# Optimization experiments

Hardware: AMD Instinct MI355X
Metric: run time of the kernel (lower is better)

The kernel has to match this reference:

```python
import math
import jax, jax.numpy as jnp
import numpy as np

T, N, D = 8, 1024, 128  # num_timestamps, tot_nodes, node_input_size

def setup_inputs() -> dict:
    key = jax.random.key(0)
    k1, k2 = jax.random.split(key)
    raw_features = jax.random.normal(k1, (T, N, D), dtype=jnp.float32)
    adj = jax.random.randint(k2, (N, N), 0, 2, dtype=jnp.int32)
    return {"raw_features": raw_features, "adj": adj}

def reference(raw_features, adj):
    t, n, d = raw_features.shape
    scale = 1.0 / math.sqrt(d)
    # --- GAT: adjacency-masked self-attention per timestamp ---
    scores = jnp.einsum('tnd,tmd->tnm', raw_features, raw_features) * scale  # [T,N,N]
    masked = jnp.where(adj[None] > 0, scores, jnp.float32(-1e12))
    attention = jax.nn.softmax(masked, axis=2)
    node_features = jnp.einsum('tnm,tmd->tnd', attention, raw_features)      # [T,N,D]
    # --- temporal scores per node ---
    spatial_features = node_features.transpose(1, 0, 2)                      # [N,T,D]
    temp_scores = jnp.einsum('ntd,nsd->nts', spatial_features, spatial_features) * scale
    spatial_weights = jax.nn.sigmoid(temp_scores)                            # [N,T,T]
    # --- repeat(N,1,1).view(N,N,T,T) == broadcast over leading axis: ST[i,j] = sw[j] ---
    ST = jnp.broadcast_to(spatial_weights[None], (n, n, t, t))               # [N,N,T,T]
    ST = ST.transpose(3, 1, 2, 0)                                            # [T,N,T,N]
    return ST.reshape(t * n, t * n)
```

## Files before the change

### kernel.cpp

```cpp
#include <hip/hip_runtime.h>
#include <hip/hip_bf16.h>
#include <math.h>

#define T 8
#define N 1024
#define D 128

constexpr float SCALE = 0.08838834764831845f;

typedef __attribute__((ext_vector_type(8))) short short8;
typedef __attribute__((ext_vector_type(4))) float floatx4;

#define MFMA16(a, b, c) __builtin_amdgcn_mfma_f32_16x16x32_bf16((a), (b), (c), 0, 0, 0)

__global__ __launch_bounds__(256) void convert_bf16(const float* __restrict__ X,
                                                    ushort* __restrict__ XB,
                                                    ushort* __restrict__ XBT_hi,
                                                    ushort* __restrict__ XBT_lo) {
    const int t  = blockIdx.y;
    const int n0 = blockIdx.x * 64;
    const int tid = threadIdx.x;

    __shared__ ushort Hi[128][66];
    __shared__ ushort Lo[128][66];

    #pragma unroll
    for (int r = 0; r < 8; ++r) {
        int idx = r * 256 + tid;
        int nl  = idx >> 5;
        int c4  = idx & 31;
        float4 v = *(const float4*)(X + ((size_t)t * N + n0 + nl) * D + c4 * 4);
        float vv[4] = {v.x, v.y, v.z, v.w};
        ushort4 o; ushort* op = (ushort*)&o;
        #pragma unroll
        for (int k = 0; k < 4; ++k) {
            __hip_bfloat16 h = __float2bfloat16(vv[k]);
            float hf = __bfloat162float(h);
            __hip_bfloat16 l = __float2bfloat16(vv[k] - hf);
            op[k] = *(ushort*)&h;
            Hi[c4 * 4 + k][nl] = *(ushort*)&h;
            Lo[c4 * 4 + k][nl] = *(ushort*)&l;
        }
        *(ushort4*)(XB + ((size_t)t * N + n0 + nl) * D + c4 * 4) = o;
    }
    __syncthreads();

    const int u  = tid & 31;
    const int dr = tid >> 5;
    #pragma unroll
    for (int p = 0; p < 16; ++p) {
        int d = p * 8 + dr;
        uint hv = *(const uint*)&Hi[d][2 * u];
        uint lv = *(const uint*)&Lo[d][2 * u];
        size_t off = ((size_t)t * D + d) * N + n0 + 2 * u;
        *(uint*)(XBT_hi + off) = hv;
        *(uint*)(XBT_lo + off) = lv;
    }
}

__global__ __launch_bounds__(256) void attn_fused(const ushort* __restrict__ XB,
                                                  const ushort* __restrict__ XBT_hi,
                                                  const ushort* __restrict__ XBT_lo,
                                                  const int* __restrict__ adj,
                                                  float* __restrict__ NF) {
    const int t  = blockIdx.y;
    const int i0 = blockIdx.x * 16;
    const int tid  = threadIdx.x;
    const int wid  = tid >> 6;
    const int lane = tid & 63;
    const int m    = lane & 15;
    const int quad = lane >> 4;
    const int jbase = wid * 256;

    __shared__ ushort Ph[16][1024];
    __shared__ ushort Plo[16][1024];
    float* red = (float*)&Ph[0][0];

    const ushort* Xt = XB + (size_t)t * N * D;

    short8 afrag[4];
    {
        const ushort* pa = Xt + (size_t)(i0 + m) * D + quad * 8;
        #pragma unroll
        for (int kq = 0; kq < 4; ++kq) afrag[kq] = *(const short8*)(pa + kq * 32);
    }

    floatx4 acc[16];
    #pragma unroll
    for (int c = 0; c < 16; ++c) acc[c] = (floatx4){0.f, 0.f, 0.f, 0.f};

    #pragma unroll
    for (int c = 0; c < 16; ++c) {
        const ushort* pb = Xt + (size_t)(jbase + 16 * c + m) * D + quad * 8;
        short8 b0 = *(const short8*)(pb);
        short8 b1 = *(const short8*)(pb + 32);
        short8 b2 = *(const short8*)(pb + 64);
        short8 b3 = *(const short8*)(pb + 96);
        acc[c] = MFMA16(afrag[0], b0, acc[c]);
        acc[c] = MFMA16(afrag[1], b1, acc[c]);
        acc[c] = MFMA16(afrag[2], b2, acc[c]);
        acc[c] = MFMA16(afrag[3], b3, acc[c]);
    }

    #pragma unroll
    for (int q = 0; q < 4; ++q) {
        const int i = i0 + quad * 4 + q;
        const int* arow = adj + (size_t)i * N + jbase + m;
        #pragma unroll
        for (int c = 0; c < 16; ++c) {
            int a = arow[16 * c];
            acc[c][q] = (a != 0) ? acc[c][q] * SCALE : -1e12f;
        }
    }

    float mx[4], inv[4];
    #pragma unroll
    for (int q = 0; q < 4; ++q) {
        float v_ = acc[0][q];
        #pragma unroll
        for (int c = 1; c < 16; ++c) v_ = fmaxf(v_, acc[c][q]);
        v_ = fmaxf(v_, __shfl_xor(v_, 1));
        v_ = fmaxf(v_, __shfl_xor(v_, 2));
        v_ = fmaxf(v_, __shfl_xor(v_, 4));
        v_ = fmaxf(v_, __shfl_xor(v_, 8));
        mx[q] = v_;
    }
    if (m == 0) {
        #pragma unroll
        for (int q = 0; q < 4; ++q) red[wid * 16 + quad * 4 + q] = mx[q];
    }
    __syncthreads();
    #pragma unroll
    for (int q = 0; q < 4; ++q) {
        int r = quad * 4 + q;
        mx[q] = fmaxf(fmaxf(red[r], red[16 + r]), fmaxf(red[32 + r], red[48 + r]));
    }

    float sm[4];
    #pragma unroll
    for (int q = 0; q < 4; ++q) {
        float s_ = 0.f;
        #pragma unroll
        for (int c = 0; c < 16; ++c) {
            float p = __expf(acc[c][q] - mx[q]);
            acc[c][q] = p;
            s_ += p;
        }
        s_ += __shfl_xor(s_, 1);
        s_ += __shfl_xor(s_, 2);
        s_ += __shfl_xor(s_, 4);
        s_ += __shfl_xor(s_, 8);
        sm[q] = s_;
    }
    if (m == 0) {
        #pragma unroll
        for (int q = 0; q < 4; ++q) red[64 + wid * 16 + quad * 4 + q] = sm[q];
    }
    __syncthreads();
    #pragma unroll
    for (int q = 0; q < 4; ++q) {
        int r = quad * 4 + q;
        inv[q] = 1.f / (red[64 + r] + red[80 + r] + red[96 + r] + red[112 + r]);
    }
    __syncthreads();

    #pragma unroll
    for (int q = 0; q < 4; ++q) {
        const int row = quad * 4 + q;
        #pragma unroll
        for (int c = 0; c < 16; ++c) {
            const int col = jbase + 16 * c + m;
            const int sc = ((((col >> 3) ^ (row & 7)) << 3) | (col & 7));
            float p = acc[c][q] * inv[q];
            __hip_bfloat16 h = __float2bfloat16(p);
            float hf = __bfloat162float(h);
            __hip_bfloat16 l = __float2bfloat16(p - hf);
            Ph[row][sc]  = *(ushort*)&h;
            Plo[row][sc] = *(ushort*)&l;
        }
    }
    __syncthreads();

    floatx4 accN[2];
    accN[0] = (floatx4){0.f, 0.f, 0.f, 0.f};
    accN[1] = (floatx4){0.f, 0.f, 0.f, 0.f};
    const int f0 = wid * 32;
    #pragma unroll 4
    for (int kq = 0; kq < 32; ++kq) {
        const int blk = (((kq * 4 + quad) ^ (m & 7)) << 3);
        short8 ah = *(const short8*)&Ph[m][blk];
        short8 al = *(const short8*)&Plo[m][blk];
        #pragma unroll
        for (int nt = 0; nt < 2; ++nt) {
            size_t off = ((size_t)t * D + f0 + nt * 16 + m) * N + kq * 32 + quad * 8;
            short8 bh = *(const short8*)(XBT_hi + off);
            short8 bl = *(const short8*)(XBT_lo + off);
            accN[nt] = MFMA16(ah, bh, accN[nt]);
            accN[nt] = MFMA16(ah, bl, accN[nt]);
            accN[nt] = MFMA16(al, bh, accN[nt]);
        }
    }

    float* NFt = NF + (size_t)t * N * D;
    #pragma unroll
    for (int nt = 0; nt < 2; ++nt)
        #pragma unroll
        for (int q = 0; q < 4; ++q)
            NFt[(size_t)(i0 + quad * 4 + q) * D + f0 + nt * 16 + m] = accN[nt][q];
}

__global__ __launch_bounds__(256) void expand_fused(const float* __restrict__ NF,
                                                    float* __restrict__ out) {
    const int row = blockIdx.x;
    const int b = row >> 10, j = row & 1023;
    const int tid = threadIdx.x;

    __shared__ float F[T][D + 4];
    __shared__ float w[T];

    {
        int a = tid >> 5, c4 = (tid & 31) * 4;
        *(float4*)(&F[a][c4]) = *(const float4*)(NF + ((size_t)a * N + j) * D + c4);
    }
    __syncthreads();

    if (tid < T) {
        float s = 0.f;
        #pragma unroll
        for (int d4 = 0; d4 < 32; ++d4) {
            float4 fa = *(const float4*)(&F[tid][d4 * 4]);
            float4 fb = *(const float4*)(&F[b][d4 * 4]);
            s += fa.x * fb.x + fa.y * fb.y + fa.z * fb.z + fa.w * fb.w;
        }
        w[tid] = 1.f / (1.f + __expf(-s * SCALE));
    }
    __syncthreads();

    floatx4* orow = (floatx4*)(out + (size_t)row * (T * N));
    #pragma unroll
    for (int a = 0; a < T; ++a) {
        float wv = w[a];
        floatx4 v = {wv, wv, wv, wv};
        __builtin_nontemporal_store(v, orow + a * 256 + tid);
    }
}

extern "C" void kernel_launch(void* const* d_in, const int* in_sizes, int n_in,
                              void* d_out, int out_size, void* d_ws, size_t ws_size,
                              hipStream_t stream) {
    const float* X   = (const float*)d_in[0];
    const int*   adj = (const int*)d_in[1];
    float* out = (float*)d_out;

    float*  NF     = (float*)d_ws;
    ushort* XB     = (ushort*)(NF + (size_t)T * N * D);
    ushort* XBT_hi = XB + (size_t)T * N * D;
    ushort* XBT_lo = XBT_hi + (size_t)T * N * D;

    convert_bf16<<<dim3(N / 64, T), 256, 0, stream>>>(X, XB, XBT_hi, XBT_lo);
    attn_fused<<<dim3(N / 16, T), 256, 0, stream>>>(XB, XBT_hi, XBT_lo, adj, NF);
    expand_fused<<<dim3(T * N), 256, 0, stream>>>(NF, out);
}
```

Before: 320.1 us.

## Pack adjacency into bitmasks and software-pipeline B-operand loads in attention

A new kernel packs the int32 adjacency matrix into 16-bit masks, so the attention kernel reads the mask as a few vector loads instead of 64 scattered int loads per thread for every timestamp. The QK^T loop double-buffers the B fragments, and the PV loop prefetches XBT hi/lo fragments three iterations ahead, issuing the first ones before the softmax. The kernel now has launch bounds allowing 2 blocks per CU. The extra register pressure from the prefetch buffers could cause spills, and the kernel adds a small launch and workspace buffer. The total time is likely dominated by the 256 MB output write in expand_fused, which limits how much the attention changes can matter.

```diff
diff --git a/kernel.cpp b/kernel.cpp
--- a/kernel.cpp
+++ b/kernel.cpp
@@ -58,11 +58,28 @@
     }
 }
 
-__global__ __launch_bounds__(256) void attn_fused(const ushort* __restrict__ XB,
-                                                  const ushort* __restrict__ XBT_hi,
-                                                  const ushort* __restrict__ XBT_lo,
-                                                  const int* __restrict__ adj,
-                                                  float* __restrict__ NF) {
+__global__ __launch_bounds__(256) void pack_adj(const int* __restrict__ adj,
+                                                ushort* __restrict__ Abits) {
+    int g = blockIdx.x * 256 + threadIdx.x;
+    int i = g >> 6, w = g & 63;
+    const int4* p4 = (const int4*)(adj + (size_t)i * N + w * 16);
+    uint m16 = 0;
+    #pragma unroll
+    for (int v4 = 0; v4 < 4; ++v4) {
+        int4 v = p4[v4];
+        m16 |= (v.x != 0 ? 1u : 0u) << (v4 * 4 + 0);
+        m16 |= (v.y != 0 ? 1u : 0u) << (v4 * 4 + 1);
+        m16 |= (v.z != 0 ? 1u : 0u) << (v4 * 4 + 2);
+        m16 |= (v.w != 0 ? 1u : 0u) << (v4 * 4 + 3);
+    }
+    Abits[g] = (ushort)m16;
+}
+
+__global__ __launch_bounds__(256, 2) void attn_fused(const ushort* __restrict__ XB,
+                                                     const ushort* __restrict__ XBT_hi,
+                                                     const ushort* __restrict__ XBT_lo,
+                                                     const ushort* __restrict__ Abits,
+                                                     float* __restrict__ NF) {
     const int t  = blockIdx.y;
     const int i0 = blockIdx.x * 16;
     const int tid  = threadIdx.x;
@@ -78,6 +95,14 @@
 
     const ushort* Xt = XB + (size_t)t * N * D;
 
+    short8 adjw[4][2];
+    #pragma unroll
+    for (int q = 0; q < 4; ++q) {
+        const ushort* ap = Abits + (size_t)(i0 + quad * 4 + q) * 64 + wid * 16;
+        adjw[q][0] = *(const short8*)ap;
+        adjw[q][1] = *(const short8*)(ap + 8);
+    }
+
     short8 afrag[4];
     {
         const ushort* pa = Xt + (size_t)(i0 + m) * D + quad * 8;
@@ -89,29 +114,57 @@
     #pragma unroll
     for (int c = 0; c < 16; ++c) acc[c] = (floatx4){0.f, 0.f, 0.f, 0.f};
 
+    short8 bfr[2][4];
+    {
+        const ushort* pb = Xt + (size_t)(jbase + m) * D + quad * 8;
+        bfr[0][0] = *(const short8*)(pb);
+        bfr[0][1] = *(const short8*)(pb + 32);
+        bfr[0][2] = *(const short8*)(pb + 64);
+        bfr[0][3] = *(const short8*)(pb + 96);
+    }
     #pragma unroll
     for (int c = 0; c < 16; ++c) {
-        const ushort* pb = Xt + (size_t)(jbase + 16 * c + m) * D + quad * 8;
-        short8 b0 = *(const short8*)(pb);
-        short8 b1 = *(const short8*)(pb + 32);
-        short8 b2 = *(const short8*)(pb + 64);
-        short8 b3 = *(const short8*)(pb + 96);
-        acc[c] = MFMA16(afrag[0], b0, acc[c]);
-        acc[c] = MFMA16(afrag[1], b1, acc[c]);
-        acc[c] = MFMA16(afrag[2], b2, acc[c]);
-        acc[c] = MFMA16(afrag[3], b3, acc[c]);
-    }
-
-    #pragma unroll
-    for (int q = 0; q < 4; ++q) {
-        const int i = i0 + quad * 4 + q;
-        const int* arow = adj + (size_t)i * N + jbase + m;
+        if (c < 15) {
+            const ushort* pb = Xt + (size_t)(jbase + 16 * (c + 1) + m) * D + quad * 8;
+            bfr[(c + 1) & 1][0] = *(const short8*)(pb);
+            bfr[(c + 1) & 1][1] = *(const short8*)(pb + 32);
+            bfr[(c + 1) & 1][2] = *(const short8*)(pb + 64);
+            bfr[(c + 1) & 1][3] = *(const short8*)(pb + 96);
+        }
+        acc[c] = MFMA16(afrag[0], bfr[c & 1][0], acc[c]);
+        acc[c] = MFMA16(afrag[1], bfr[c & 1][1], acc[c]);
+        acc[c] = MFMA16(afrag[2], bfr[c & 1][2], acc[c]);
+        acc[c] = MFMA16(afrag[3], bfr[c & 1][3], acc[c]);
+    }
+
+    #pragma unroll
+    for (int q = 0; q < 4; ++q) {
         #pragma unroll
         for (int c = 0; c < 16; ++c) {
-            int a = arow[16 * c];
-            acc[c][q] = (a != 0) ? acc[c][q] * SCALE : -1e12f;
-        }
-    }
+            int aw = (ushort)((c < 8) ? adjw[q][0][c] : adjw[q][1][c - 8]);
+            acc[c][q] = ((aw >> m) & 1) ? acc[c][q] * SCALE : -1e12f;
+        }
+    }
+
+    const ushort* rowh[2];
+    const ushort* rowl[2];
+    const int f0 = wid * 32;
+    #pragma unroll
+    for (int nt = 0; nt < 2; ++nt) {
+        size_t rb = ((size_t)t * D + f0 + nt * 16 + m) * N;
+        rowh[nt] = XBT_hi + rb;
+        rowl[nt] = XBT_lo + rb;
+    }
+    short8 pfh[4][2], pfl[4][2];
+#define PF(kq_)                                                                  \
+    {                                                                            \
+        const int off_ = (kq_) * 32 + quad * 8;                                  \
+        pfh[(kq_) & 3][0] = *(const short8*)(rowh[0] + off_);                    \
+        pfh[(kq_) & 3][1] = *(const short8*)(rowh[1] + off_);                    \
+        pfl[(kq_) & 3][0] = *(const short8*)(rowl[0] + off_);                    \
+        pfl[(kq_) & 3][1] = *(const short8*)(rowl[1] + off_);                    \
+    }
+    PF(0); PF(1); PF(2);
 
     float mx[4], inv[4];
     #pragma unroll
@@ -184,22 +237,20 @@
     floatx4 accN[2];
     accN[0] = (floatx4){0.f, 0.f, 0.f, 0.f};
     accN[1] = (floatx4){0.f, 0.f, 0.f, 0.f};
-    const int f0 = wid * 32;
-    #pragma unroll 4
+    #pragma unroll
     for (int kq = 0; kq < 32; ++kq) {
+        if (kq < 29) PF(kq + 3);
         const int blk = (((kq * 4 + quad) ^ (m & 7)) << 3);
         short8 ah = *(const short8*)&Ph[m][blk];
         short8 al = *(const short8*)&Plo[m][blk];
         #pragma unroll
         for (int nt = 0; nt < 2; ++nt) {
-            size_t off = ((size_t)t * D + f0 + nt * 16 + m) * N + kq * 32 + quad * 8;
-            short8 bh = *(const short8*)(XBT_hi + off);
-            short8 bl = *(const short8*)(XBT_lo + off);
-            accN[nt] = MFMA16(ah, bh, accN[nt]);
-            accN[nt] = MFMA16(ah, bl, accN[nt]);
-            accN[nt] = MFMA16(al, bh, accN[nt]);
-        }
-    }
+            accN[nt] = MFMA16(ah, pfh[kq & 3][nt], accN[nt]);
+            accN[nt] = MFMA16(ah, pfl[kq & 3][nt], accN[nt]);
+            accN[nt] = MFMA16(al, pfh[kq & 3][nt], accN[nt]);
+        }
+    }
+#undef PF
 
     float* NFt = NF + (size_t)t * N * D;
     #pragma unroll
@@ -256,8 +307,10 @@
     ushort* XB     = (ushort*)(NF + (size_t)T * N * D);
     ushort* XBT_hi = XB + (size_t)T * N * D;
     ushort* XBT_lo = XBT_hi + (size_t)T * N * D;
+    ushort* Abits  = XBT_lo + (size_t)T * N * D;
 
     convert_bf16<<<dim3(N / 64, T), 256, 0, stream>>>(X, XB, XBT_hi, XBT_lo);
-    attn_fused<<<dim3(N / 16, T), 256, 0, stream>>>(XB, XBT_hi, XBT_lo, adj, NF);
+    pack_adj<<<dim3(N * 64 / 256), 256, 0, stream>>>(adj, Abits);
+    attn_fused<<<dim3(N / 16, T), 256, 0, stream>>>(XB, XBT_hi, XBT_lo, Abits, NF);
     expand_fused<<<dim3(T * N), 256, 0, stream>>>(NF, out);
 }
```

New measurement: 322.6 us. About the same (+0.8%).
